# Optimization experiments

Measured on AMD Instinct MI355X. Metric: run time of the kernel, lower is better.

## Reference

```python
import jax, jax.numpy as jnp
import numpy as np

N, B, FD, D, MSG, SCN, H, FFN = 2048, 16, 128, 32, 32, 16, 4, 64
HD = D // H


def _lin(k, o, i, scale=0.05):
    kw, kb = jax.random.split(k)
    return (jax.random.normal(kw, (o, i), jnp.float32) * scale,
            jax.random.normal(kb, (o,), jnp.float32) * scale)


def setup_inputs() -> dict:
    key = jax.random.key(0)
    ks = jax.random.split(key, 24)
    inp = {}
    inp['src'] = jax.random.randint(ks[0], (B,), 0, N)
    inp['dst'] = jax.random.randint(ks[1], (B,), 0, N)
    inp['edge_feat'] = jax.random.normal(ks[2], (B, 3), jnp.float32)
    inp['timestamps'] = jax.random.uniform(ks[3], (B,), dtype=jnp.float32)
    inp['node_features'] = jax.random.normal(ks[4], (N, FD), jnp.float32)
    inp['adj'] = jnp.zeros((N, N), jnp.float32)  # unused: assume_identity_adj=True
    inp['memory'] = jax.random.normal(ks[5], (N, D), jnp.float32) * 0.1
    inp['W_emb'], inp['b_emb'] = _lin(ks[6], D, FD)
    inp['Wqkv'], inp['bqkv'] = _lin(ks[7], 3 * D, D)
    inp['Wo'], inp['bo'] = _lin(ks[8], D, D)
    inp['g1'] = jnp.ones((D,), jnp.float32); inp['be1'] = jnp.zeros((D,), jnp.float32)
    inp['g2'] = jnp.ones((D,), jnp.float32); inp['be2'] = jnp.zeros((D,), jnp.float32)
    inp['W_f1'], inp['b_f1'] = _lin(ks[9], FFN, D)
    inp['W_f2'], inp['b_f2'] = _lin(ks[10], D, FFN)
    inp['W_scn'], inp['b_scn'] = _lin(ks[11], SCN, D)
    inp['g_scn'] = jnp.ones((SCN,), jnp.float32); inp['be_scn'] = jnp.zeros((SCN,), jnp.float32)
    inp['W_e1'], inp['b_e1'] = _lin(ks[12], 32, 2 * SCN)
    inp['W_e2'], inp['b_e2'] = _lin(ks[13], 16, 32)
    inp['W_e3'], inp['b_e3'] = _lin(ks[14], 1, 16)
    inp['gru_Wih'], inp['gru_bih'] = _lin(ks[15], 3 * D, MSG)
    inp['gru_Whh'], inp['gru_bhh'] = _lin(ks[16], 3 * D, D)
    inp['W_m1'], inp['b_m1'] = _lin(ks[17], MSG, 2 * D + 3)
    inp['W_m2'], inp['b_m2'] = _lin(ks[18], MSG, MSG)
    return inp


def _ln(x, g, b):
    mu = x.mean(-1, keepdims=True)
    var = ((x - mu) ** 2).mean(-1, keepdims=True)
    return (x - mu) * jax.lax.rsqrt(var + 1e-5) * g + b


def _gru(x, h, Wih, Whh, bih, bhh):
    # torch.nn.GRUCell semantics
    gi = x @ Wih.T + bih
    gh = h @ Whh.T + bhh
    ir, iz, i_n = jnp.split(gi, 3, -1)
    hr, hz, h_n = jnp.split(gh, 3, -1)
    r = jax.nn.sigmoid(ir + hr)
    z = jax.nn.sigmoid(iz + hz)
    n = jnp.tanh(i_n + r * h_n)
    return (1.0 - z) * n + z * h


def _update_memory(memory, src, dst, edge_feat,
                   gru_Wih, gru_Whh, gru_bih, gru_bhh, W_m1, b_m1, W_m2, b_m2):
    # messages computed from pre-update memory (as in torch source)
    msg_in = jnp.concatenate([memory[src], memory[dst], edge_feat], axis=1)  # [B, 2D+3]
    messages = jax.nn.relu(msg_in @ W_m1.T + b_m1) @ W_m2.T + b_m2           # [B, MSG]

    def step(mem, inp):
        s, d, m = inp
        hs = _gru(m, mem[s], gru_Wih, gru_Whh, gru_bih, gru_bhh)
        mem = mem.at[s].set(hs)
        hd = _gru(m, mem[d], gru_Wih, gru_Whh, gru_bih, gru_bhh)  # sees updated mem if d==s earlier
        mem = mem.at[d].set(hd)
        return mem, None

    new_mem, _ = jax.lax.scan(step, memory, (src, dst, messages))
    return new_mem


def _edge_logits(node_features, src, dst,
                 W_emb, b_emb, Wqkv, bqkv, Wo, bo, g1, be1, g2, be2,
                 W_f1, b_f1, W_f2, b_f2, W_scn, b_scn, g_scn, be_scn,
                 W_e1, b_e1, W_e2, b_e2, W_e3, b_e3):
    x0 = node_features @ W_emb.T + b_emb                      # [N, D]
    x = jnp.broadcast_to(x0[None], (B, N, D))                 # [B, N, D]
    # --- Graph transformer layer (MHA, eval mode: dropout = identity) ---
    qkv = x @ Wqkv.T + bqkv                                   # [B, N, 3D]
    q, k, v = jnp.split(qkv, 3, -1)
    q = q.reshape(B, N, H, HD)
    k = k.reshape(B, N, H, HD)
    v = v.reshape(B, N, H, HD)
    scores = jnp.einsum('bqhd,bkhd->bhqk', q, k) / np.sqrt(HD)
    attn = jax.nn.softmax(scores, axis=-1)
    ao = jnp.einsum('bhqk,bkhd->bqhd', attn, v).reshape(B, N, D)
    ao = ao @ Wo.T + bo
    x = _ln(x + ao, g1, be1)
    ffn = jax.nn.gelu(x @ W_f1.T + b_f1, approximate=False) @ W_f2.T + b_f2
    x = _ln(x + ffn, g2, be2)
    # --- SCN layer (identity adjacency assumed) ---
    s_out = jax.nn.relu(_ln(x @ W_scn.T + b_scn, g_scn, be_scn))  # [B, N, SCN]
    bi = jnp.arange(B)
    src_emb = s_out[bi, src]
    dst_emb = s_out[bi, dst]
    h = jnp.concatenate([src_emb, dst_emb], axis=-1)
    h = jax.nn.relu(h @ W_e1.T + b_e1)
    h = jax.nn.relu(h @ W_e2.T + b_e2)
    return (h @ W_e3.T + b_e3).squeeze(-1)                    # [B]


def reference(src, dst, edge_feat, timestamps, node_features, adj, memory,
              W_emb, b_emb, Wqkv, bqkv, Wo, bo, g1, be1, g2, be2,
              W_f1, b_f1, W_f2, b_f2, W_scn, b_scn, g_scn, be_scn,
              W_e1, b_e1, W_e2, b_e2, W_e3, b_e3,
              gru_Wih, gru_bih, gru_Whh, gru_bhh, W_m1, b_m1, W_m2, b_m2):
    new_mem = _update_memory(memory, src, dst, edge_feat,
                             gru_Wih, gru_Whh, gru_bih, gru_bhh,
                             W_m1, b_m1, W_m2, b_m2)
    edge_logit = _edge_logits(node_features, src, dst,
                              W_emb, b_emb, Wqkv, bqkv, Wo, bo, g1, be1, g2, be2,
                              W_f1, b_f1, W_f2, b_f2, W_scn, b_scn, g_scn, be_scn,
                              W_e1, b_e1, W_e2, b_e2, W_e3, b_e3)
    return edge_logit, new_mem
```

## Files before the change

kernel.cpp:

```cpp
#include <hip/hip_runtime.h>
#include <math.h>

#define NN   2048
#define BB   16

#define WS_X0   0
#define WS_QT   65536
#define WS_KT   131072
#define WS_VT   196608
#define WS_PART 262144
#define WS_GI   268800

#define B_BO    0
#define B_G1    32
#define B_BE1   64
#define B_G2    96
#define B_BE2   128
#define B_BF1   160
#define B_BF2   224
#define B_BSCN  256
#define B_GSCN  272
#define B_BESCN 288
#define B_BE1E  304
#define B_BE2E  336
#define B_WE3   352
#define B_BE3   368

__device__ __forceinline__ float sigmoidf_(float x) { return 1.0f / (1.0f + __expf(-x)); }
__device__ __forceinline__ float tanhf_(float x) {
    float ex = __expf(2.0f * x);
    return 1.0f - 2.0f / (ex + 1.0f);
}
__device__ __forceinline__ float dot4_(float4 a, float4 b) {
    return a.x*b.x + a.y*b.y + a.z*b.z + a.w*b.w;
}

__global__ __launch_bounds__(256) void k1_embed_qkv_msg(
    const float* __restrict__ nf, const float* __restrict__ Wemb, const float* __restrict__ bemb,
    const float* __restrict__ Wqkv, const float* __restrict__ bqkv,
    const float* __restrict__ mem, const int* __restrict__ src, const int* __restrict__ dst,
    const float* __restrict__ ef,
    const float* __restrict__ Wm1, const float* __restrict__ bm1,
    const float* __restrict__ Wm2, const float* __restrict__ bm2,
    const float* __restrict__ Wih, const float* __restrict__ bih,
    float* __restrict__ ws, float* __restrict__ out)
{
    __shared__ float We_s[32 * 130];
    __shared__ float nf_s[8 * 130];
    __shared__ float x0_s[8 * 33];
    __shared__ float Wq_s[96 * 33];
    __shared__ __align__(16) float Wm1_s[2144];
    __shared__ float Wm2_s[32 * 33];
    __shared__ float Wih_s[96 * 33];
    __shared__ float min_s[67];
    __shared__ float mr_s[32];
    __shared__ float msg_s[32];

    const int t = threadIdx.x, bx = blockIdx.x;
    const bool domsg = (bx < 16);

    float4 rA[4], rB[3], rC;
    #pragma unroll
    for (int k = 0; k < 4; ++k) rA[k] = ((const float4*)Wemb)[t + 256 * k];
    #pragma unroll
    for (int k = 0; k < 3; ++k) rB[k] = ((const float4*)Wqkv)[t + 256 * k];
    rC = ((const float4*)nf)[bx * 256 + t];

    float4 rm1[3], rm2v, rih[3];
    float rminv = 0.f;
    if (domsg) {
        #pragma unroll
        for (int k = 0; k < 3; ++k) {
            int idx = t + 256 * k;
            rm1[k] = (idx < 536) ? ((const float4*)Wm1)[idx] : make_float4(0,0,0,0);
        }
        rm2v = ((const float4*)Wm2)[t];
        #pragma unroll
        for (int k = 0; k < 3; ++k) rih[k] = ((const float4*)Wih)[t + 256 * k];
        if (t < 67) {
            const int e = bx;
            rminv = (t < 32) ? mem[src[e] * 32 + t]
                  : (t < 64) ? mem[dst[e] * 32 + (t - 32)]
                             : ef[e * 3 + (t - 64)];
        }
    }

    if (bx >= 16 && bx < 80) {
        int g = (bx - 16) * 256 + t;
        ((float4*)(out + 16))[g] = ((const float4*)mem)[g];
    }

    #pragma unroll
    for (int k = 0; k < 4; ++k) {
        int idx = t + 256 * k;
        int r = idx >> 5, c = (idx & 31) * 4;
        We_s[r * 130 + c] = rA[k].x; We_s[r * 130 + c + 1] = rA[k].y;
        We_s[r * 130 + c + 2] = rA[k].z; We_s[r * 130 + c + 3] = rA[k].w;
    }
    #pragma unroll
    for (int k = 0; k < 3; ++k) {
        int idx = t + 256 * k;
        int r = idx >> 3, c = (idx & 7) * 4;
        Wq_s[r * 33 + c] = rB[k].x; Wq_s[r * 33 + c + 1] = rB[k].y;
        Wq_s[r * 33 + c + 2] = rB[k].z; Wq_s[r * 33 + c + 3] = rB[k].w;
    }
    {
        int r = t >> 5, c = (t & 31) * 4;
        nf_s[r * 130 + c] = rC.x; nf_s[r * 130 + c + 1] = rC.y;
        nf_s[r * 130 + c + 2] = rC.z; nf_s[r * 130 + c + 3] = rC.w;
    }
    if (domsg) {
        #pragma unroll
        for (int k = 0; k < 3; ++k) {
            int idx = t + 256 * k;
            if (idx < 536) ((float4*)Wm1_s)[idx] = rm1[k];
        }
        { int r = t >> 3, c = (t & 7) * 4;
          Wm2_s[r * 33 + c] = rm2v.x; Wm2_s[r * 33 + c + 1] = rm2v.y;
          Wm2_s[r * 33 + c + 2] = rm2v.z; Wm2_s[r * 33 + c + 3] = rm2v.w; }
        #pragma unroll
        for (int k = 0; k < 3; ++k) {
            int idx = t + 256 * k;
            int r = idx >> 3, c = (idx & 7) * 4;
            Wih_s[r * 33 + c] = rih[k].x; Wih_s[r * 33 + c + 1] = rih[k].y;
            Wih_s[r * 33 + c + 2] = rih[k].z; Wih_s[r * 33 + c + 3] = rih[k].w;
        }
        if (t < 67) min_s[t] = rminv;
    }
    __syncthreads();

    const int j = t >> 5, o = t & 31;
    const int n = bx * 8 + j;

    float acc = bemb[o];
    {
        const float2* Wr = (const float2*)&We_s[o * 130];
        const float2* Nr = (const float2*)&nf_s[j * 130];
        float sx = 0.f, sy = 0.f;
        #pragma unroll 16
        for (int i = 0; i < 64; ++i) {
            float2 w = Wr[i], x = Nr[i];
            sx += w.x * x.x; sy += w.y * x.y;
        }
        acc += sx + sy;
    }
    x0_s[j * 33 + o] = acc;
    ws[WS_X0 + n * 32 + o] = acc;
    if (domsg && t < 32) {
        float a1 = bm1[t];
        for (int i = 0; i < 67; ++i) a1 += Wm1_s[t * 67 + i] * min_s[i];
        mr_s[t] = fmaxf(a1, 0.f);
    }
    __syncthreads();

    #pragma unroll
    for (int c = 0; c < 3; ++c) {
        int oo = c * 32 + o;
        float a2 = bqkv[oo];
        #pragma unroll 8
        for (int i = 0; i < 32; ++i) a2 += Wq_s[oo * 33 + i] * x0_s[j * 33 + i];
        int h = o >> 3, d = o & 7;
        float* base = ws + (c == 0 ? WS_QT : (c == 1 ? WS_KT : WS_VT));
        base[h * 16384 + n * 8 + d] = a2;
    }
    if (domsg && t < 32) {
        float a2 = bm2[t];
        #pragma unroll 8
        for (int i = 0; i < 32; ++i) a2 += Wm2_s[t * 33 + i] * mr_s[i];
        msg_s[t] = a2;
    }
    __syncthreads();

    if (domsg && t < 96) {
        float a3 = bih[t];
        #pragma unroll 8
        for (int i = 0; i < 32; ++i) a3 += Wih_s[t * 33 + i] * msg_s[i];
        ws[WS_GI + bx * 96 + t] = a3;
    }
}

__global__ __launch_bounds__(256) void k2_attn(
    const int* __restrict__ src, const int* __restrict__ dst,
    float* __restrict__ ws)
{
    const int t = threadIdx.x, bx = blockIdx.x;
    const int s  = bx >> 2;
    const int ks = bx & 3;
    const int h  = t >> 6;
    const int l  = t & 63;

    const int e = s >> 1;
    const int n = (s & 1) ? dst[e] : src[e];

    const float* qg = ws + WS_QT + h * 16384 + n * 8;
    const float4 qa  = *(const float4*)qg;
    const float4 qb4 = *(const float4*)(qg + 4);
    const float* kbase = ws + WS_KT + h * 16384;
    const float* vbase = ws + WS_VT + h * 16384;

    float4 oa = make_float4(0.f, 0.f, 0.f, 0.f);
    float4 ob = make_float4(0.f, 0.f, 0.f, 0.f);
    float ssum = 0.f;
    const float scale = 0.35355339059327373f;

    #pragma unroll
    for (int i = 0; i < 8; ++i) {
        const int key = ks * 512 + i * 64 + l;
        const float4 ka = *(const float4*)(kbase + key * 8);
        const float4 kb = *(const float4*)(kbase + key * 8 + 4);
        const float sc = (dot4_(qa, ka) + dot4_(qb4, kb)) * scale;
        const float p = __expf(sc);
        ssum += p;
        const float4 va = *(const float4*)(vbase + key * 8);
        const float4 vb = *(const float4*)(vbase + key * 8 + 4);
        oa.x += p * va.x; oa.y += p * va.y; oa.z += p * va.z; oa.w += p * va.w;
        ob.x += p * vb.x; ob.y += p * vb.y; ob.z += p * vb.z; ob.w += p * vb.w;
    }

    #pragma unroll
    for (int m = 1; m <= 32; m <<= 1) {
        ssum += __shfl_xor(ssum, m);
        oa.x += __shfl_xor(oa.x, m); oa.y += __shfl_xor(oa.y, m);
        oa.z += __shfl_xor(oa.z, m); oa.w += __shfl_xor(oa.w, m);
        ob.x += __shfl_xor(ob.x, m); ob.y += __shfl_xor(ob.y, m);
        ob.z += __shfl_xor(ob.z, m); ob.w += __shfl_xor(ob.w, m);
    }
    if (l == 0) {
        float* p = ws + WS_PART + ((s * 4 + h) * 4 + ks) * 12;
        *(float4*)p       = oa;
        *(float4*)(p + 4) = ob;
        p[8] = ssum;
    }
}

__global__ __launch_bounds__(256, 1) void k34_post_scan(
    const int* __restrict__ src, const int* __restrict__ dst,
    const float* __restrict__ mem,
    const float* __restrict__ Wo, const float* __restrict__ bo,
    const float* __restrict__ g1, const float* __restrict__ be1,
    const float* __restrict__ Wf1, const float* __restrict__ bf1,
    const float* __restrict__ Wf2, const float* __restrict__ bf2,
    const float* __restrict__ g2, const float* __restrict__ be2,
    const float* __restrict__ Wscn, const float* __restrict__ bscn,
    const float* __restrict__ gscn, const float* __restrict__ bescn,
    const float* __restrict__ Whh, const float* __restrict__ bhh,
    const float* __restrict__ We1, const float* __restrict__ be1e,
    const float* __restrict__ We2, const float* __restrict__ be2e,
    const float* __restrict__ We3, const float* __restrict__ be3,
    float* __restrict__ ws, float* __restrict__ out)
{
    __shared__ float Wo_s[32 * 33];
    __shared__ float Wf1_s[64 * 33];
    __shared__ float Wf2_s[32 * 65];
    __shared__ float Ws_s[16 * 33];
    __shared__ float We1_s[32 * 33];
    __shared__ float We2_s[16 * 33];
    __shared__ float arow[32 * 33];
    __shared__ float x1s[32 * 33];
    __shared__ float fs[32 * 65];
    __shared__ float gi_s[16 * 97];
    __shared__ __align__(16) float slots[32 * 36];
    __shared__ float bias_s[384];
    __shared__ int nid_s[32], prev_s[32], round_s[32], last_s[32];
    __shared__ int list_s[32], cnt_s, maxr_s;

    const int t = threadIdx.x;
    const int j0 = t >> 5, o = t & 31;
    const int l = t & 63, w = t >> 6;
    const bool lowhalf = (l < 32);

    float4 w1[8], w2[8], w3[8];
    {
        const int r2 = lowhalf ? l + 64 : l - 32;
        const int r3 = l + 32;
        #pragma unroll
        for (int c = 0; c < 8; ++c) {
            w1[c] = ((const float4*)Whh)[l * 8 + c];
            w2[c] = ((const float4*)Whh)[r2 * 8 + c];
            w3[c] = ((const float4*)Whh)[r3 * 8 + c];
        }
    }
    const float b1 = bhh[l], b2 = bhh[lowhalf ? l + 64 : l - 32], b3 = bhh[l + 32];

    float4 rWo, rF1a, rF1b, rF2a, rF2b, rE1, rWs, rE2, rG0, rG1;
    rWo  = ((const float4*)Wo)[t];
    rF1a = ((const float4*)Wf1)[t]; rF1b = ((const float4*)Wf1)[t + 256];
    rF2a = ((const float4*)Wf2)[t]; rF2b = ((const float4*)Wf2)[t + 256];
    rE1  = ((const float4*)We1)[t];
    rG0  = ((const float4*)(ws + WS_GI))[t];
    if (t < 128) {
        rWs = ((const float4*)Wscn)[t];
        rE2 = ((const float4*)We2)[t];
        rG1 = ((const float4*)(ws + WS_GI))[t + 256];
    }
    if (t < 32) {
        bias_s[B_BO + t]   = bo[t];
        bias_s[B_G1 + t]   = g1[t];
        bias_s[B_BE1 + t]  = be1[t];
        bias_s[B_G2 + t]   = g2[t];
        bias_s[B_BE2 + t]  = be2[t];
        bias_s[B_BF1 + t]  = bf1[t];
        bias_s[B_BF1 + 32 + t] = bf1[32 + t];
        bias_s[B_BF2 + t]  = bf2[t];
        bias_s[B_BE1E + t] = be1e[t];
        nid_s[t] = (t & 1) ? dst[t >> 1] : src[t >> 1];
    }
    if (t < 16) {
        bias_s[B_BSCN + t]  = bscn[t];
        bias_s[B_GSCN + t]  = gscn[t];
        bias_s[B_BESCN + t] = bescn[t];
        bias_s[B_BE2E + t]  = be2e[t];
        bias_s[B_WE3 + t]   = We3[t];
    }
    if (t == 0) bias_s[B_BE3] = be3[0];

    { int r = t >> 3, c = (t & 7) * 4;
      Wo_s[r * 33 + c] = rWo.x; Wo_s[r * 33 + c + 1] = rWo.y;
      Wo_s[r * 33 + c + 2] = rWo.z; Wo_s[r * 33 + c + 3] = rWo.w;
      We1_s[r * 33 + c] = rE1.x; We1_s[r * 33 + c + 1] = rE1.y;
      We1_s[r * 33 + c + 2] = rE1.z; We1_s[r * 33 + c + 3] = rE1.w;
      Wf1_s[r * 33 + c] = rF1a.x; Wf1_s[r * 33 + c + 1] = rF1a.y;
      Wf1_s[r * 33 + c + 2] = rF1a.z; Wf1_s[r * 33 + c + 3] = rF1a.w;
      int r2 = (t + 256) >> 3, c2 = ((t + 256) & 7) * 4;
      Wf1_s[r2 * 33 + c2] = rF1b.x; Wf1_s[r2 * 33 + c2 + 1] = rF1b.y;
      Wf1_s[r2 * 33 + c2 + 2] = rF1b.z; Wf1_s[r2 * 33 + c2 + 3] = rF1b.w; }
    { int r = t >> 4, c = (t & 15) * 4;
      Wf2_s[r * 65 + c] = rF2a.x; Wf2_s[r * 65 + c + 1] = rF2a.y;
      Wf2_s[r * 65 + c + 2] = rF2a.z; Wf2_s[r * 65 + c + 3] = rF2a.w;
      int r2 = (t + 256) >> 4, c2 = ((t + 256) & 15) * 4;
      Wf2_s[r2 * 65 + c2] = rF2b.x; Wf2_s[r2 * 65 + c2 + 1] = rF2b.y;
      Wf2_s[r2 * 65 + c2 + 2] = rF2b.z; Wf2_s[r2 * 65 + c2 + 3] = rF2b.w; }
    { int f = 4 * t, e = f / 96, off = f - e * 96;
      gi_s[e * 97 + off] = rG0.x; gi_s[e * 97 + off + 1] = rG0.y;
      gi_s[e * 97 + off + 2] = rG0.z; gi_s[e * 97 + off + 3] = rG0.w; }
    if (t < 128) {
        int r = t >> 3, c = (t & 7) * 4;
        Ws_s[r * 33 + c] = rWs.x; Ws_s[r * 33 + c + 1] = rWs.y;
        Ws_s[r * 33 + c + 2] = rWs.z; Ws_s[r * 33 + c + 3] = rWs.w;
        We2_s[r * 33 + c] = rE2.x; We2_s[r * 33 + c + 1] = rE2.y;
        We2_s[r * 33 + c + 2] = rE2.z; We2_s[r * 33 + c + 3] = rE2.w;
        int f = 4 * (t + 256), e2 = f / 96, off = f - e2 * 96;
        gi_s[e2 * 97 + off] = rG1.x; gi_s[e2 * 97 + off + 1] = rG1.y;
        gi_s[e2 * 97 + off + 2] = rG1.z; gi_s[e2 * 97 + off + 3] = rG1.w;
    }

    float x0v[4];
    #pragma unroll
    for (int si = 0; si < 4; ++si) {
        const int jj = si * 8 + j0;
        const int ej = jj >> 1;
        const int n = (jj & 1) ? dst[ej] : src[ej];
        const int h = o >> 3, d = o & 7;
        float num = 0.f, den = 0.f;
        #pragma unroll
        for (int ks = 0; ks < 4; ++ks) {
            const float* p = ws + WS_PART + ((jj * 4 + h) * 4 + ks) * 12;
            num += p[d];
            den += p[8];
        }
        arow[jj * 33 + o] = num / den;
        x0v[si] = ws[WS_X0 + n * 32 + o];
    }
    __syncthreads();

    if (t < 32) {
        const int me = nid_s[t];
        int pv = -1, rd = 0;
        for (int j2 = 0; j2 < t; ++j2) if (nid_s[j2] == me) { pv = j2; ++rd; }
        prev_s[t] = pv; round_s[t] = rd;
        int isl = 1;
        for (int j2 = t + 1; j2 < 32; ++j2) if (nid_s[j2] == me) { isl = 0; break; }
        last_s[t] = isl;
        int mr = rd;
        #pragma unroll
        for (int m = 16; m >= 1; m >>= 1) mr = max(mr, __shfl_xor(mr, m, 32));
        if (t == 0) maxr_s = mr;
    }
    #pragma unroll
    for (int k = 0; k < 4; ++k) {
        int j2 = j0 + 8 * k;
        slots[j2 * 36 + o] = mem[nid_s[j2] * 32 + o];
    }

    #pragma unroll
    for (int si = 0; si < 4; ++si) {
        const int jj = si * 8 + j0;
        float a = bias_s[B_BO + o];
        #pragma unroll 8
        for (int i = 0; i < 32; ++i) a += Wo_s[o * 33 + i] * arow[jj * 33 + i];
        float t1 = x0v[si] + a;
        float mu = t1;
        #pragma unroll
        for (int m = 16; m >= 1; m >>= 1) mu += __shfl_xor(mu, m, 32);
        mu *= (1.f / 32.f);
        float dv = t1 - mu;
        float var = dv * dv;
        #pragma unroll
        for (int m = 16; m >= 1; m >>= 1) var += __shfl_xor(var, m, 32);
        var *= (1.f / 32.f);
        x1s[jj * 33 + o] = dv * rsqrtf(var + 1e-5f) * bias_s[B_G1 + o] + bias_s[B_BE1 + o];
    }
    __syncthreads();

    #pragma unroll
    for (int si = 0; si < 4; ++si) {
        const int jj = si * 8 + j0;
        #pragma unroll
        for (int c = 0; c < 2; ++c) {
            int oo = c * 32 + o;
            float f = bias_s[B_BF1 + oo];
            #pragma unroll 8
            for (int i = 0; i < 32; ++i) f += Wf1_s[oo * 33 + i] * x1s[jj * 33 + i];
            fs[jj * 65 + oo] = 0.5f * f * (1.f + erff(f * 0.70710678118654752f));
        }
    }
    __syncthreads();

    #pragma unroll
    for (int si = 0; si < 4; ++si) {
        const int jj = si * 8 + j0;
        float f2 = bias_s[B_BF2 + o];
        #pragma unroll 8
        for (int i = 0; i < 64; ++i) f2 += Wf2_s[o * 65 + i] * fs[jj * 65 + i];
        float t2 = x1s[jj * 33 + o] + f2;
        float mu2 = t2;
        #pragma unroll
        for (int m = 16; m >= 1; m >>= 1) mu2 += __shfl_xor(mu2, m, 32);
        mu2 *= (1.f / 32.f);
        float dv2 = t2 - mu2;
        float var2 = dv2 * dv2;
        #pragma unroll
        for (int m = 16; m >= 1; m >>= 1) var2 += __shfl_xor(var2, m, 32);
        var2 *= (1.f / 32.f);
        x1s[jj * 33 + o] = dv2 * rsqrtf(var2 + 1e-5f) * bias_s[B_G2 + o] + bias_s[B_BE2 + o];
    }
    __syncthreads();

    if (o < 16) {
        #pragma unroll
        for (int si = 0; si < 4; ++si) {
            const int jj = si * 8 + j0;
            float sc = bias_s[B_BSCN + o];
            #pragma unroll 8
            for (int i = 0; i < 32; ++i) sc += Ws_s[o * 33 + i] * x1s[jj * 33 + i];
            float m16 = sc;
            #pragma unroll
            for (int m = 8; m >= 1; m >>= 1) m16 += __shfl_xor(m16, m, 16);
            m16 *= (1.f / 16.f);
            float d16 = sc - m16;
            float v16 = d16 * d16;
            #pragma unroll
            for (int m = 8; m >= 1; m >>= 1) v16 += __shfl_xor(v16, m, 16);
            v16 *= (1.f / 16.f);
            float sv = d16 * rsqrtf(v16 + 1e-5f) * bias_s[B_GSCN + o] + bias_s[B_BESCN + o];
            arow[(jj >> 1) * 33 + (jj & 1) * 16 + o] = fmaxf(sv, 0.f);
        }
    }
    __syncthreads();

    #pragma unroll
    for (int k = 0; k < 2; ++k) {
        int e = j0 + 8 * k;
        float acc = bias_s[B_BE1E + o];
        #pragma unroll 8
        for (int i = 0; i < 32; ++i) acc += We1_s[o * 33 + i] * arow[e * 33 + i];
        fs[e * 33 + o] = fmaxf(acc, 0.f);
    }
    __syncthreads();

    {
        int e = t >> 4, o2 = t & 15;
        float acc = bias_s[B_BE2E + o2];
        #pragma unroll 8
        for (int i = 0; i < 32; ++i) acc += We2_s[o2 * 33 + i] * fs[e * 33 + i];
        fs[600 + e * 17 + o2] = fmaxf(acc, 0.f);
    }
    __syncthreads();

    if (t < 16) {
        float acc = bias_s[B_BE3];
        #pragma unroll
        for (int i = 0; i < 16; ++i) acc += bias_s[B_WE3 + i] * fs[600 + t * 17 + i];
        out[t] = acc;
    }

    const int maxr = maxr_s;
    for (int r = 0; r <= maxr; ++r) {
        if (t < 64) {
            bool act = (t < 32) && (round_s[t] == r);
            unsigned long long mask = __ballot(act);
            if (act) {
                int pos = __popcll(mask & ((1ull << t) - 1ull));
                list_s[pos] = t;
            }
            if (t == 0) cnt_s = (int)__popcll(mask);
        }
        __syncthreads();
        const int cnt = cnt_s;
        for (int pi = w; 2 * pi < cnt; pi += 4) {
            const int sA = list_s[2 * pi];
            const bool doB = (2 * pi + 1 < cnt);
            const int sB = doB ? list_s[2 * pi + 1] : sA;
            const int inA = (prev_s[sA] < 0) ? sA : prev_s[sA];
            const int inB = (prev_s[sB] < 0) ? sB : prev_s[sB];
            float acc1 = b1, acc2 = b2, acc3 = b3;
            #pragma unroll
            for (int c = 0; c < 8; ++c) {
                const float4 hs4 = *(const float4*)&slots[inA * 36 + 4 * c];
                const float4 hd4 = *(const float4*)&slots[inB * 36 + 4 * c];
                acc1 += dot4_(w1[c], hs4);
                const float4 hm = lowhalf ? hs4 : hd4;
                acc2 += dot4_(w2[c], hm);
                acc3 += dot4_(w3[c], hd4);
            }
            const float shv = __shfl_xor(lowhalf ? acc3 : acc1, 32);
            const float hr = lowhalf ? acc1 : acc2;
            const float hz = shv;
            const float hn = lowhalf ? acc2 : acc3;
            const int sX = lowhalf ? sA : sB;
            const int eX = sX >> 1;
            const float ir  = gi_s[eX * 97 + o];
            const float iz  = gi_s[eX * 97 + 32 + o];
            const float inn = gi_s[eX * 97 + 64 + o];
            const float rr = sigmoidf_(ir + hr);
            const float z = sigmoidf_(iz + hz);
            const float nn = tanhf_(inn + rr * hn);
            const float hold = slots[(lowhalf ? inA : inB) * 36 + o];
            const float hnew = (1.f - z) * nn + z * hold;
            if (lowhalf || doB) slots[sX * 36 + o] = hnew;
        }
        __syncthreads();
    }

    #pragma unroll
    for (int k = 0; k < 4; ++k) {
        int j2 = j0 + 8 * k;
        if (last_s[j2]) out[16 + nid_s[j2] * 32 + o] = slots[j2 * 36 + o];
    }
}

extern "C" void kernel_launch(void* const* d_in, const int* in_sizes, int n_in,
                              void* d_out, int out_size, void* d_ws, size_t ws_size,
                              hipStream_t stream)
{
    (void)in_sizes; (void)n_in; (void)out_size; (void)ws_size;
    const int*   src   = (const int*)d_in[0];
    const int*   dst   = (const int*)d_in[1];
    const float* ef    = (const float*)d_in[2];
    const float* nf    = (const float*)d_in[4];
    const float* mem   = (const float*)d_in[6];
    const float* Wemb  = (const float*)d_in[7];
    const float* bemb  = (const float*)d_in[8];
    const float* Wqkv  = (const float*)d_in[9];
    const float* bqkv  = (const float*)d_in[10];
    const float* Wo    = (const float*)d_in[11];
    const float* bo    = (const float*)d_in[12];
    const float* g1    = (const float*)d_in[13];
    const float* be1   = (const float*)d_in[14];
    const float* g2    = (const float*)d_in[15];
    const float* be2   = (const float*)d_in[16];
    const float* Wf1   = (const float*)d_in[17];
    const float* bf1   = (const float*)d_in[18];
    const float* Wf2   = (const float*)d_in[19];
    const float* bf2   = (const float*)d_in[20];
    const float* Wscn  = (const float*)d_in[21];
    const float* bscn  = (const float*)d_in[22];
    const float* gscn  = (const float*)d_in[23];
    const float* bescn = (const float*)d_in[24];
    const float* We1   = (const float*)d_in[25];
    const float* be1e  = (const float*)d_in[26];
    const float* We2   = (const float*)d_in[27];
    const float* be2e  = (const float*)d_in[28];
    const float* We3   = (const float*)d_in[29];
    const float* be3   = (const float*)d_in[30];
    const float* Wih   = (const float*)d_in[31];
    const float* bih   = (const float*)d_in[32];
    const float* Whh   = (const float*)d_in[33];
    const float* bhh   = (const float*)d_in[34];
    const float* Wm1   = (const float*)d_in[35];
    const float* bm1   = (const float*)d_in[36];
    const float* Wm2   = (const float*)d_in[37];
    const float* bm2   = (const float*)d_in[38];
    float* out = (float*)d_out;
    float* ws  = (float*)d_ws;

    hipLaunchKernelGGL(k1_embed_qkv_msg, dim3(256), dim3(256), 0, stream,
        nf, Wemb, bemb, Wqkv, bqkv, mem, src, dst, ef, Wm1, bm1, Wm2, bm2, Wih, bih, ws, out);
    hipLaunchKernelGGL(k2_attn, dim3(128), dim3(256), 0, stream, src, dst, ws);
    hipLaunchKernelGGL(k34_post_scan, dim3(1), dim3(256), 0, stream,
        src, dst, mem, Wo, bo, g1, be1, Wf1, bf1, Wf2, bf2, g2, be2,
        Wscn, bscn, gscn, bescn, Whh, bhh, We1, be1e, We2, be2e, We3, be3, ws, out);
}
```

Before: 174.2 us.

## Read weights straight into registers instead of staging through shared memory

```diff
diff --git a/kernel.cpp b/kernel.cpp
--- a/kernel.cpp
+++ b/kernel.cpp
@@ -10,21 +10,6 @@
 #define WS_VT   196608
 #define WS_PART 262144
 #define WS_GI   268800
-
-#define B_BO    0
-#define B_G1    32
-#define B_BE1   64
-#define B_G2    96
-#define B_BE2   128
-#define B_BF1   160
-#define B_BF2   224
-#define B_BSCN  256
-#define B_GSCN  272
-#define B_BESCN 288
-#define B_BE1E  304
-#define B_BE2E  336
-#define B_WE3   352
-#define B_BE3   368
 
 __device__ __forceinline__ float sigmoidf_(float x) { return 1.0f / (1.0f + __expf(-x)); }
 __device__ __forceinline__ float tanhf_(float x) {
@@ -249,18 +234,10 @@
     const float* __restrict__ We3, const float* __restrict__ be3,
     float* __restrict__ ws, float* __restrict__ out)
 {
-    __shared__ float Wo_s[32 * 33];
-    __shared__ float Wf1_s[64 * 33];
-    __shared__ float Wf2_s[32 * 65];
-    __shared__ float Ws_s[16 * 33];
-    __shared__ float We1_s[32 * 33];
-    __shared__ float We2_s[16 * 33];
     __shared__ float arow[32 * 33];
     __shared__ float x1s[32 * 33];
     __shared__ float fs[32 * 65];
-    __shared__ float gi_s[16 * 97];
     __shared__ __align__(16) float slots[32 * 36];
-    __shared__ float bias_s[384];
     __shared__ int nid_s[32], prev_s[32], round_s[32], last_s[32];
     __shared__ int list_s[32], cnt_s, maxr_s;
 
@@ -270,82 +247,19 @@
     const bool lowhalf = (l < 32);
 
     float4 w1[8], w2[8], w3[8];
-    {
-        const int r2 = lowhalf ? l + 64 : l - 32;
-        const int r3 = l + 32;
-        #pragma unroll
-        for (int c = 0; c < 8; ++c) {
-            w1[c] = ((const float4*)Whh)[l * 8 + c];
-            w2[c] = ((const float4*)Whh)[r2 * 8 + c];
-            w3[c] = ((const float4*)Whh)[r3 * 8 + c];
-        }
-    }
-    const float b1 = bhh[l], b2 = bhh[lowhalf ? l + 64 : l - 32], b3 = bhh[l + 32];
-
-    float4 rWo, rF1a, rF1b, rF2a, rF2b, rE1, rWs, rE2, rG0, rG1;
-    rWo  = ((const float4*)Wo)[t];
-    rF1a = ((const float4*)Wf1)[t]; rF1b = ((const float4*)Wf1)[t + 256];
-    rF2a = ((const float4*)Wf2)[t]; rF2b = ((const float4*)Wf2)[t + 256];
-    rE1  = ((const float4*)We1)[t];
-    rG0  = ((const float4*)(ws + WS_GI))[t];
-    if (t < 128) {
-        rWs = ((const float4*)Wscn)[t];
-        rE2 = ((const float4*)We2)[t];
-        rG1 = ((const float4*)(ws + WS_GI))[t + 256];
-    }
-    if (t < 32) {
-        bias_s[B_BO + t]   = bo[t];
-        bias_s[B_G1 + t]   = g1[t];
-        bias_s[B_BE1 + t]  = be1[t];
-        bias_s[B_G2 + t]   = g2[t];
-        bias_s[B_BE2 + t]  = be2[t];
-        bias_s[B_BF1 + t]  = bf1[t];
-        bias_s[B_BF1 + 32 + t] = bf1[32 + t];
-        bias_s[B_BF2 + t]  = bf2[t];
-        bias_s[B_BE1E + t] = be1e[t];
-        nid_s[t] = (t & 1) ? dst[t >> 1] : src[t >> 1];
-    }
-    if (t < 16) {
-        bias_s[B_BSCN + t]  = bscn[t];
-        bias_s[B_GSCN + t]  = gscn[t];
-        bias_s[B_BESCN + t] = bescn[t];
-        bias_s[B_BE2E + t]  = be2e[t];
-        bias_s[B_WE3 + t]   = We3[t];
-    }
-    if (t == 0) bias_s[B_BE3] = be3[0];
-
-    { int r = t >> 3, c = (t & 7) * 4;
-      Wo_s[r * 33 + c] = rWo.x; Wo_s[r * 33 + c + 1] = rWo.y;
-      Wo_s[r * 33 + c + 2] = rWo.z; Wo_s[r * 33 + c + 3] = rWo.w;
-      We1_s[r * 33 + c] = rE1.x; We1_s[r * 33 + c + 1] = rE1.y;
-      We1_s[r * 33 + c + 2] = rE1.z; We1_s[r * 33 + c + 3] = rE1.w;
-      Wf1_s[r * 33 + c] = rF1a.x; Wf1_s[r * 33 + c + 1] = rF1a.y;
-      Wf1_s[r * 33 + c + 2] = rF1a.z; Wf1_s[r * 33 + c + 3] = rF1a.w;
-      int r2 = (t + 256) >> 3, c2 = ((t + 256) & 7) * 4;
-      Wf1_s[r2 * 33 + c2] = rF1b.x; Wf1_s[r2 * 33 + c2 + 1] = rF1b.y;
-      Wf1_s[r2 * 33 + c2 + 2] = rF1b.z; Wf1_s[r2 * 33 + c2 + 3] = rF1b.w; }
-    { int r = t >> 4, c = (t & 15) * 4;
-      Wf2_s[r * 65 + c] = rF2a.x; Wf2_s[r * 65 + c + 1] = rF2a.y;
-      Wf2_s[r * 65 + c + 2] = rF2a.z; Wf2_s[r * 65 + c + 3] = rF2a.w;
-      int r2 = (t + 256) >> 4, c2 = ((t + 256) & 15) * 4;
-      Wf2_s[r2 * 65 + c2] = rF2b.x; Wf2_s[r2 * 65 + c2 + 1] = rF2b.y;
-      Wf2_s[r2 * 65 + c2 + 2] = rF2b.z; Wf2_s[r2 * 65 + c2 + 3] = rF2b.w; }
-    { int f = 4 * t, e = f / 96, off = f - e * 96;
-      gi_s[e * 97 + off] = rG0.x; gi_s[e * 97 + off + 1] = rG0.y;
-      gi_s[e * 97 + off + 2] = rG0.z; gi_s[e * 97 + off + 3] = rG0.w; }
-    if (t < 128) {
-        int r = t >> 3, c = (t & 7) * 4;
-        Ws_s[r * 33 + c] = rWs.x; Ws_s[r * 33 + c + 1] = rWs.y;
-        Ws_s[r * 33 + c + 2] = rWs.z; Ws_s[r * 33 + c + 3] = rWs.w;
-        We2_s[r * 33 + c] = rE2.x; We2_s[r * 33 + c + 1] = rE2.y;
-        We2_s[r * 33 + c + 2] = rE2.z; We2_s[r * 33 + c + 3] = rE2.w;
-        int f = 4 * (t + 256), e2 = f / 96, off = f - e2 * 96;
-        gi_s[e2 * 97 + off] = rG1.x; gi_s[e2 * 97 + off + 1] = rG1.y;
-        gi_s[e2 * 97 + off + 2] = rG1.z; gi_s[e2 * 97 + off + 3] = rG1.w;
-    }
-
-    float x0v[4];
-    #pragma unroll
+    const int r2 = lowhalf ? l + 64 : l - 32;
+    const int r3 = l + 32;
+    #pragma unroll
+    for (int c = 0; c < 8; ++c) {
+        w1[c] = ((const float4*)Whh)[l * 8 + c];
+        w2[c] = ((const float4*)Whh)[r2 * 8 + c];
+        w3[c] = ((const float4*)Whh)[r3 * 8 + c];
+    }
+    const float b1 = bhh[l], b2 = bhh[r2], b3 = bhh[r3];
+
+    if (t < 32) nid_s[t] = (t & 1) ? dst[t >> 1] : src[t >> 1];
+
+    #pragma unroll 1
     for (int si = 0; si < 4; ++si) {
         const int jj = si * 8 + j0;
         const int ej = jj >> 1;
@@ -359,7 +273,7 @@
             den += p[8];
         }
         arow[jj * 33 + o] = num / den;
-        x0v[si] = ws[WS_X0 + n * 32 + o];
+        fs[jj * 65 + o] = ws[WS_X0 + n * 32 + o];
     }
     __syncthreads();
 
@@ -382,67 +296,113 @@
         slots[j2 * 36 + o] = mem[nid_s[j2] * 32 + o];
     }
 
-    #pragma unroll
-    for (int si = 0; si < 4; ++si) {
-        const int jj = si * 8 + j0;
-        float a = bias_s[B_BO + o];
-        #pragma unroll 8
-        for (int i = 0; i < 32; ++i) a += Wo_s[o * 33 + i] * arow[jj * 33 + i];
-        float t1 = x0v[si] + a;
-        float mu = t1;
-        #pragma unroll
-        for (int m = 16; m >= 1; m >>= 1) mu += __shfl_xor(mu, m, 32);
-        mu *= (1.f / 32.f);
-        float dv = t1 - mu;
-        float var = dv * dv;
-        #pragma unroll
-        for (int m = 16; m >= 1; m >>= 1) var += __shfl_xor(var, m, 32);
-        var *= (1.f / 32.f);
-        x1s[jj * 33 + o] = dv * rsqrtf(var + 1e-5f) * bias_s[B_G1 + o] + bias_s[B_BE1 + o];
-    }
-    __syncthreads();
-
-    #pragma unroll
-    for (int si = 0; si < 4; ++si) {
-        const int jj = si * 8 + j0;
-        #pragma unroll
-        for (int c = 0; c < 2; ++c) {
-            int oo = c * 32 + o;
-            float f = bias_s[B_BF1 + oo];
-            #pragma unroll 8
-            for (int i = 0; i < 32; ++i) f += Wf1_s[oo * 33 + i] * x1s[jj * 33 + i];
-            fs[jj * 65 + oo] = 0.5f * f * (1.f + erff(f * 0.70710678118654752f));
-        }
-    }
-    __syncthreads();
-
-    #pragma unroll
-    for (int si = 0; si < 4; ++si) {
-        const int jj = si * 8 + j0;
-        float f2 = bias_s[B_BF2 + o];
-        #pragma unroll 8
-        for (int i = 0; i < 64; ++i) f2 += Wf2_s[o * 65 + i] * fs[jj * 65 + i];
-        float t2 = x1s[jj * 33 + o] + f2;
-        float mu2 = t2;
-        #pragma unroll
-        for (int m = 16; m >= 1; m >>= 1) mu2 += __shfl_xor(mu2, m, 32);
-        mu2 *= (1.f / 32.f);
-        float dv2 = t2 - mu2;
-        float var2 = dv2 * dv2;
-        #pragma unroll
-        for (int m = 16; m >= 1; m >>= 1) var2 += __shfl_xor(var2, m, 32);
-        var2 *= (1.f / 32.f);
-        x1s[jj * 33 + o] = dv2 * rsqrtf(var2 + 1e-5f) * bias_s[B_G2 + o] + bias_s[B_BE2 + o];
-    }
-    __syncthreads();
-
-    if (o < 16) {
-        #pragma unroll
+    {
+        float4 wv[8];
+        #pragma unroll
+        for (int c = 0; c < 8; ++c) wv[c] = ((const float4*)(Wo + o * 32))[c];
+        const float bv = bo[o], gv = g1[o], bev = be1[o];
+        #pragma unroll 1
         for (int si = 0; si < 4; ++si) {
             const int jj = si * 8 + j0;
-            float sc = bias_s[B_BSCN + o];
-            #pragma unroll 8
-            for (int i = 0; i < 32; ++i) sc += Ws_s[o * 33 + i] * x1s[jj * 33 + i];
+            float a = bv;
+            #pragma unroll
+            for (int c = 0; c < 8; ++c) {
+                a = fmaf(wv[c].x, arow[jj * 33 + 4 * c],     a);
+                a = fmaf(wv[c].y, arow[jj * 33 + 4 * c + 1], a);
+                a = fmaf(wv[c].z, arow[jj * 33 + 4 * c + 2], a);
+                a = fmaf(wv[c].w, arow[jj * 33 + 4 * c + 3], a);
+            }
+            float t1 = fs[jj * 65 + o] + a;
+            float mu = t1;
+            #pragma unroll
+            for (int m = 16; m >= 1; m >>= 1) mu += __shfl_xor(mu, m, 32);
+            mu *= (1.f / 32.f);
+            float dv = t1 - mu;
+            float var = dv * dv;
+            #pragma unroll
+            for (int m = 16; m >= 1; m >>= 1) var += __shfl_xor(var, m, 32);
+            var *= (1.f / 32.f);
+            x1s[jj * 33 + o] = dv * rsqrtf(var + 1e-5f) * gv + bev;
+        }
+    }
+    __syncthreads();
+
+    {
+        float4 wa[8], wb[8];
+        #pragma unroll
+        for (int c = 0; c < 8; ++c) {
+            wa[c] = ((const float4*)(Wf1 + o * 32))[c];
+            wb[c] = ((const float4*)(Wf1 + (o + 32) * 32))[c];
+        }
+        const float ba = bf1[o], bb = bf1[o + 32];
+        #pragma unroll 1
+        for (int si = 0; si < 4; ++si) {
+            const int jj = si * 8 + j0;
+            float f0 = ba, f1 = bb;
+            #pragma unroll
+            for (int c = 0; c < 8; ++c) {
+                const float xa = x1s[jj * 33 + 4 * c];
+                const float xb = x1s[jj * 33 + 4 * c + 1];
+                const float xc = x1s[jj * 33 + 4 * c + 2];
+                const float xd = x1s[jj * 33 + 4 * c + 3];
+                f0 = fmaf(wa[c].x, xa, f0); f0 = fmaf(wa[c].y, xb, f0);
+                f0 = fmaf(wa[c].z, xc, f0); f0 = fmaf(wa[c].w, xd, f0);
+                f1 = fmaf(wb[c].x, xa, f1); f1 = fmaf(wb[c].y, xb, f1);
+                f1 = fmaf(wb[c].z, xc, f1); f1 = fmaf(wb[c].w, xd, f1);
+            }
+            fs[jj * 65 + o]      = 0.5f * f0 * (1.f + erff(f0 * 0.70710678118654752f));
+            fs[jj * 65 + 32 + o] = 0.5f * f1 * (1.f + erff(f1 * 0.70710678118654752f));
+        }
+    }
+    __syncthreads();
+
+    {
+        float4 wv[16];
+        #pragma unroll
+        for (int c = 0; c < 16; ++c) wv[c] = ((const float4*)(Wf2 + o * 64))[c];
+        const float bv = bf2[o], gv = g2[o], bev = be2[o];
+        #pragma unroll 1
+        for (int si = 0; si < 4; ++si) {
+            const int jj = si * 8 + j0;
+            float f2 = bv;
+            #pragma unroll
+            for (int c = 0; c < 16; ++c) {
+                f2 = fmaf(wv[c].x, fs[jj * 65 + 4 * c],     f2);
+                f2 = fmaf(wv[c].y, fs[jj * 65 + 4 * c + 1], f2);
+                f2 = fmaf(wv[c].z, fs[jj * 65 + 4 * c + 2], f2);
+                f2 = fmaf(wv[c].w, fs[jj * 65 + 4 * c + 3], f2);
+            }
+            float t2 = x1s[jj * 33 + o] + f2;
+            float mu2 = t2;
+            #pragma unroll
+            for (int m = 16; m >= 1; m >>= 1) mu2 += __shfl_xor(mu2, m, 32);
+            mu2 *= (1.f / 32.f);
+            float dv2 = t2 - mu2;
+            float var2 = dv2 * dv2;
+            #pragma unroll
+            for (int m = 16; m >= 1; m >>= 1) var2 += __shfl_xor(var2, m, 32);
+            var2 *= (1.f / 32.f);
+            x1s[jj * 33 + o] = dv2 * rsqrtf(var2 + 1e-5f) * gv + bev;
+        }
+    }
+    __syncthreads();
+
+    if (o < 16) {
+        float4 wv[8];
+        #pragma unroll
+        for (int c = 0; c < 8; ++c) wv[c] = ((const float4*)(Wscn + o * 32))[c];
+        const float bv = bscn[o], gv = gscn[o], bev = bescn[o];
+        #pragma unroll 1
+        for (int si = 0; si < 4; ++si) {
+            const int jj = si * 8 + j0;
+            float sc = bv;
+            #pragma unroll
+            for (int c = 0; c < 8; ++c) {
+                sc = fmaf(wv[c].x, x1s[jj * 33 + 4 * c],     sc);
+                sc = fmaf(wv[c].y, x1s[jj * 33 + 4 * c + 1], sc);
+                sc = fmaf(wv[c].z, x1s[jj * 33 + 4 * c + 2], sc);
+                sc = fmaf(wv[c].w, x1s[jj * 33 + 4 * c + 3], sc);
+            }
             float m16 = sc;
             #pragma unroll
             for (int m = 8; m >= 1; m >>= 1) m16 += __shfl_xor(m16, m, 16);
@@ -452,35 +412,63 @@
             #pragma unroll
             for (int m = 8; m >= 1; m >>= 1) v16 += __shfl_xor(v16, m, 16);
             v16 *= (1.f / 16.f);
-            float sv = d16 * rsqrtf(v16 + 1e-5f) * bias_s[B_GSCN + o] + bias_s[B_BESCN + o];
+            float sv = d16 * rsqrtf(v16 + 1e-5f) * gv + bev;
             arow[(jj >> 1) * 33 + (jj & 1) * 16 + o] = fmaxf(sv, 0.f);
         }
     }
     __syncthreads();
 
-    #pragma unroll
-    for (int k = 0; k < 2; ++k) {
-        int e = j0 + 8 * k;
-        float acc = bias_s[B_BE1E + o];
-        #pragma unroll 8
-        for (int i = 0; i < 32; ++i) acc += We1_s[o * 33 + i] * arow[e * 33 + i];
-        fs[e * 33 + o] = fmaxf(acc, 0.f);
-    }
-    __syncthreads();
-
-    {
-        int e = t >> 4, o2 = t & 15;
-        float acc = bias_s[B_BE2E + o2];
-        #pragma unroll 8
-        for (int i = 0; i < 32; ++i) acc += We2_s[o2 * 33 + i] * fs[e * 33 + i];
+    {
+        float4 wv[8];
+        #pragma unroll
+        for (int c = 0; c < 8; ++c) wv[c] = ((const float4*)(We1 + o * 32))[c];
+        const float bv = be1e[o];
+        #pragma unroll 1
+        for (int k = 0; k < 2; ++k) {
+            int e = j0 + 8 * k;
+            float acc = bv;
+            #pragma unroll
+            for (int c = 0; c < 8; ++c) {
+                acc = fmaf(wv[c].x, arow[e * 33 + 4 * c],     acc);
+                acc = fmaf(wv[c].y, arow[e * 33 + 4 * c + 1], acc);
+                acc = fmaf(wv[c].z, arow[e * 33 + 4 * c + 2], acc);
+                acc = fmaf(wv[c].w, arow[e * 33 + 4 * c + 3], acc);
+            }
+            fs[e * 33 + o] = fmaxf(acc, 0.f);
+        }
+    }
+    __syncthreads();
+
+    {
+        const int e = t >> 4, o2 = t & 15;
+        float4 wv[8];
+        #pragma unroll
+        for (int c = 0; c < 8; ++c) wv[c] = ((const float4*)(We2 + o2 * 32))[c];
+        float acc = be2e[o2];
+        #pragma unroll
+        for (int c = 0; c < 8; ++c) {
+            acc = fmaf(wv[c].x, fs[e * 33 + 4 * c],     acc);
+            acc = fmaf(wv[c].y, fs[e * 33 + 4 * c + 1], acc);
+            acc = fmaf(wv[c].z, fs[e * 33 + 4 * c + 2], acc);
+            acc = fmaf(wv[c].w, fs[e * 33 + 4 * c + 3], acc);
+        }
+        __syncthreads();
         fs[600 + e * 17 + o2] = fmaxf(acc, 0.f);
     }
     __syncthreads();
 
     if (t < 16) {
-        float acc = bias_s[B_BE3];
-        #pragma unroll
-        for (int i = 0; i < 16; ++i) acc += bias_s[B_WE3 + i] * fs[600 + t * 17 + i];
+        float4 w3a = ((const float4*)We3)[0], w3b = ((const float4*)We3)[1];
+        float4 w3c = ((const float4*)We3)[2], w3d = ((const float4*)We3)[3];
+        float acc = be3[0];
+        acc = fmaf(w3a.x, fs[600 + t * 17 + 0], acc);  acc = fmaf(w3a.y, fs[600 + t * 17 + 1], acc);
+        acc = fmaf(w3a.z, fs[600 + t * 17 + 2], acc);  acc = fmaf(w3a.w, fs[600 + t * 17 + 3], acc);
+        acc = fmaf(w3b.x, fs[600 + t * 17 + 4], acc);  acc = fmaf(w3b.y, fs[600 + t * 17 + 5], acc);
+        acc = fmaf(w3b.z, fs[600 + t * 17 + 6], acc);  acc = fmaf(w3b.w, fs[600 + t * 17 + 7], acc);
+        acc = fmaf(w3c.x, fs[600 + t * 17 + 8], acc);  acc = fmaf(w3c.y, fs[600 + t * 17 + 9], acc);
+        acc = fmaf(w3c.z, fs[600 + t * 17 + 10], acc); acc = fmaf(w3c.w, fs[600 + t * 17 + 11], acc);
+        acc = fmaf(w3d.x, fs[600 + t * 17 + 12], acc); acc = fmaf(w3d.y, fs[600 + t * 17 + 13], acc);
+        acc = fmaf(w3d.z, fs[600 + t * 17 + 14], acc); acc = fmaf(w3d.w, fs[600 + t * 17 + 15], acc);
         out[t] = acc;
     }
 
@@ -497,12 +485,18 @@
         }
         __syncthreads();
         const int cnt = cnt_s;
+        #pragma unroll 1
         for (int pi = w; 2 * pi < cnt; pi += 4) {
             const int sA = list_s[2 * pi];
             const bool doB = (2 * pi + 1 < cnt);
             const int sB = doB ? list_s[2 * pi + 1] : sA;
             const int inA = (prev_s[sA] < 0) ? sA : prev_s[sA];
             const int inB = (prev_s[sB] < 0) ? sB : prev_s[sB];
+            const int sX = lowhalf ? sA : sB;
+            const int eX = sX >> 1;
+            const float ir  = ws[WS_GI + eX * 96 + o];
+            const float iz  = ws[WS_GI + eX * 96 + 32 + o];
+            const float inn = ws[WS_GI + eX * 96 + 64 + o];
             float acc1 = b1, acc2 = b2, acc3 = b3;
             #pragma unroll
             for (int c = 0; c < 8; ++c) {
@@ -517,11 +511,6 @@
             const float hr = lowhalf ? acc1 : acc2;
             const float hz = shv;
             const float hn = lowhalf ? acc2 : acc3;
-            const int sX = lowhalf ? sA : sB;
-            const int eX = sX >> 1;
-            const float ir  = gi_s[eX * 97 + o];
-            const float iz  = gi_s[eX * 97 + 32 + o];
-            const float inn = gi_s[eX * 97 + 64 + o];
             const float rr = sigmoidf_(ir + hr);
             const float z = sigmoidf_(iz + hz);
             const float nn = tanhf_(inn + rr * hn);
```

Result: slower. 178.0 us (+2.2%).
